# Optimization experiments

Hardware: AMD Instinct MI355X
Metric: run time of the kernel (lower is better)

Reference implementation:

```python
import jax, jax.numpy as jnp
import numpy as np

N_NODES = 100000
N_EDGES = 3200000
F_IN = 256
HIDDEN = 16
N_CLASSES = 32


def setup_inputs() -> dict:
    key = jax.random.key(0)
    ks = jax.random.split(key, 9)
    x = jax.random.normal(ks[0], (N_NODES, F_IN), dtype=jnp.float32)
    edge_index = jax.random.randint(ks[1], (2, N_EDGES), 0, N_NODES)
    edge_attr = jax.random.uniform(ks[2], (N_EDGES, 1), dtype=jnp.float32)
    s1 = 1.0 / np.sqrt(F_IN)
    W1 = jax.random.normal(ks[3], (2, F_IN, HIDDEN), dtype=jnp.float32) * s1
    root1 = jax.random.normal(ks[4], (F_IN, HIDDEN), dtype=jnp.float32) * s1
    bias1 = jnp.zeros((HIDDEN,), dtype=jnp.float32)
    s2 = 1.0 / np.sqrt(HIDDEN)
    W2 = jax.random.normal(ks[5], (2, HIDDEN, N_CLASSES), dtype=jnp.float32) * s2
    root2 = jax.random.normal(ks[6], (HIDDEN, N_CLASSES), dtype=jnp.float32) * s2
    bias2 = jnp.zeros((N_CLASSES,), dtype=jnp.float32)
    return {"x": x, "edge_attr": edge_attr, "W1": W1, "root1": root1,
            "bias1": bias1, "W2": W2, "root2": root2, "bias2": bias2,
            "edge_index": edge_index}


def spline_conv(x, src, dst, u, W, root, bias):
    """SplineConv, dim=1, kernel_size=2, degree=1, open spline, aggr='mean'.

    With K=2 and degree-1 open splines, v = u*(K-1) = u, so the B-spline basis
    per edge is simply ((1-u), u) over kernel weights W[0], W[1].
    """
    n = x.shape[0]
    # Node-level GEMMs once (cheaper than per-edge F_IN-dim gathers): [2, N, out]
    xs = jnp.einsum('nf,kfo->kno', x, W)
    # Per-edge basis-weighted message from source nodes: [E, out]
    msg = (1.0 - u)[:, None] * xs[0, src] + u[:, None] * xs[1, src]
    agg = jax.ops.segment_sum(msg, dst, num_segments=n)
    cnt = jax.ops.segment_sum(jnp.ones((dst.shape[0],), x.dtype), dst,
                              num_segments=n)
    return agg / jnp.maximum(cnt, 1.0)[:, None] + x @ root + bias


def reference(x, edge_attr, W1, root1, bias1, W2, root2, bias2, edge_index):
    src, dst = edge_index[0], edge_index[1]
    u = jnp.clip(edge_attr[:, 0], 0.0, 1.0)  # pseudo coords in [0, 1]
    # dropout with training=False is identity (eval-mode reference)
    h = jax.nn.elu(spline_conv(x, src, dst, u, W1, root1, bias1))
    out = spline_conv(h, src, dst, u, W2, root2, bias2)
    return jax.nn.log_softmax(out, axis=1)
```

## Files before the change

kernel.cpp:

```cpp
#include <hip/hip_runtime.h>
#include <hip/hip_fp16.h>
#include <math.h>

#define NN 100000
#define NE 3200000
#define FIN 256
#define HID 16
#define NC 32
#define NBUK 782
#define CAP 5120
#define SC_BLOCKS 250
#define SC_TILE 12800
#define SC_EPT 13
#define SK 20

typedef __attribute__((ext_vector_type(8))) short short8;
typedef __attribute__((ext_vector_type(4))) float f32x4;
typedef union { uint4 u; short8 s; } U8;

#define RU(r) ((float)((r) >> 24) * (1.f / 255.f))

__global__ __launch_bounds__(256) void k_prepB(
    const float* __restrict__ W1, const float* __restrict__ root1,
    uint4* __restrict__ Bpk)
{
    int idx = blockIdx.x * 256 + threadIdx.x;
    if (idx >= 1536) return;
    int c = idx & 15, kc = (idx >> 4) & 31, t = idx >> 9;
    unsigned hi[8], lo[8];
    #pragma unroll
    for (int e = 0; e < 8; ++e) {
        int k = kc * 8 + e;
        float v;
        if (t == 0)      v = W1[k * 16 + c];
        else if (t == 1) v = W1[FIN * 16 + k * 16 + c];
        else             v = root1[k * 16 + c];
        unsigned u = __float_as_uint(v);
        unsigned h = u & 0xFFFF0000u;
        float lf = v - __uint_as_float(h);
        hi[e] = h;
        lo[e] = __float_as_uint(lf) & 0xFFFF0000u;
    }
    uint4 H, L;
    H.x = (hi[0] >> 16) | hi[1];  H.y = (hi[2] >> 16) | hi[3];
    H.z = (hi[4] >> 16) | hi[5];  H.w = (hi[6] >> 16) | hi[7];
    L.x = (lo[0] >> 16) | lo[1];  L.y = (lo[2] >> 16) | lo[3];
    L.z = (lo[4] >> 16) | lo[5];  L.w = (lo[6] >> 16) | lo[7];
    Bpk[(size_t)idx * 2]     = H;
    Bpk[(size_t)idx * 2 + 1] = L;
}

__global__ __launch_bounds__(256) void k_gemm1(
    const float* __restrict__ x, const uint4* __restrict__ Bpk,
    const float* __restrict__ bias1,
    __half2* __restrict__ xs1p, __half2* __restrict__ r1h)
{
    int wid = (blockIdx.x << 2) + (threadIdx.x >> 6);
    if (wid >= NN / 16) return;
    int lane = threadIdx.x & 63;
    int c = lane & 15, kcl = lane >> 4;
    int n0 = wid * 16;

    const float* xr = x + (size_t)(n0 + c) * FIN + kcl * 8;
    f32x4 acc0 = {0.f, 0.f, 0.f, 0.f};
    f32x4 acc1 = {0.f, 0.f, 0.f, 0.f};
    f32x4 acc2 = {0.f, 0.f, 0.f, 0.f};

    #define PACK(f0, f1, HO, LO) {                                     \
        unsigned u0 = __float_as_uint(f0), u1 = __float_as_uint(f1);   \
        unsigned h0 = u0 & 0xFFFF0000u, h1 = u1 & 0xFFFF0000u;         \
        HO = (h0 >> 16) | h1;                                          \
        float l0 = (f0) - __uint_as_float(h0);                         \
        float l1 = (f1) - __uint_as_float(h1);                         \
        LO = (__float_as_uint(l0) >> 16) |                             \
             (__float_as_uint(l1) & 0xFFFF0000u); }

    #pragma unroll
    for (int s = 0; s < 8; ++s) {
        float4 a0 = *(const float4*)(xr + s * 32);
        float4 a1 = *(const float4*)(xr + s * 32 + 4);
        U8 ahi, alo;
        PACK(a0.x, a0.y, ahi.u.x, alo.u.x)
        PACK(a0.z, a0.w, ahi.u.y, alo.u.y)
        PACK(a1.x, a1.y, ahi.u.z, alo.u.z)
        PACK(a1.z, a1.w, ahi.u.w, alo.u.w)

        const uint4* bp = Bpk + ((size_t)((s * 4 + kcl) * 16 + c)) * 2;
        U8 bh0, bl0, bh1, bl1, bh2, bl2;
        bh0.u = bp[0];     bl0.u = bp[1];
        bh1.u = bp[1024];  bl1.u = bp[1025];
        bh2.u = bp[2048];  bl2.u = bp[2049];

        acc0 = __builtin_amdgcn_mfma_f32_16x16x32_bf16(ahi.s, bh0.s, acc0, 0, 0, 0);
        acc0 = __builtin_amdgcn_mfma_f32_16x16x32_bf16(alo.s, bh0.s, acc0, 0, 0, 0);
        acc0 = __builtin_amdgcn_mfma_f32_16x16x32_bf16(ahi.s, bl0.s, acc0, 0, 0, 0);
        acc1 = __builtin_amdgcn_mfma_f32_16x16x32_bf16(ahi.s, bh1.s, acc1, 0, 0, 0);
        acc1 = __builtin_amdgcn_mfma_f32_16x16x32_bf16(alo.s, bh1.s, acc1, 0, 0, 0);
        acc1 = __builtin_amdgcn_mfma_f32_16x16x32_bf16(ahi.s, bl1.s, acc1, 0, 0, 0);
        acc2 = __builtin_amdgcn_mfma_f32_16x16x32_bf16(ahi.s, bh2.s, acc2, 0, 0, 0);
        acc2 = __builtin_amdgcn_mfma_f32_16x16x32_bf16(alo.s, bh2.s, acc2, 0, 0, 0);
        acc2 = __builtin_amdgcn_mfma_f32_16x16x32_bf16(ahi.s, bl2.s, acc2, 0, 0, 0);
    }
    #undef PACK

    #pragma unroll
    for (int r = 0; r < 4; ++r) {
        int n = n0 + kcl * 4 + r;
        xs1p[(size_t)n * 16 + c] = __floats2half2_rn(acc0[r], acc1[r]);
    }
    float b = bias1[c];
    #pragma unroll
    for (int r = 0; r < 4; ++r) {
        int n = n0 + kcl * 4 + r;
        float v = acc2[r] + b;
        float vo = __shfl_xor(v, 1, 64);
        if (!(c & 1))
            r1h[(size_t)n * 8 + (c >> 1)] = __floats2half2_rn(v, vo);
    }
}

__global__ __launch_bounds__(1024) void k_binscatter(
    const int* __restrict__ ei, const float* __restrict__ ea,
    int* __restrict__ gcnt, unsigned* __restrict__ rec)
{
    __shared__ unsigned sbuf[SC_TILE];
    __shared__ int cnt[NBUK], gb[NBUK], cur[NBUK];
    __shared__ int ss[1024];
    int t = threadIdx.x;
    if (t < NBUK) cnt[t] = 0;
    __syncthreads();

    int e0 = blockIdx.x * SC_TILE;
    int   dl[SC_EPT];
    int   sl[SC_EPT];
    float ul[SC_EPT];
    #pragma unroll
    for (int k = 0; k < SC_EPT; ++k) {
        int i = t + k * 1024;
        if (i < SC_TILE) {
            dl[k] = ei[NE + e0 + i];
            sl[k] = ei[e0 + i];
            ul[k] = ea[e0 + i];
            atomicAdd(&cnt[dl[k] >> 7], 1);
        }
    }
    __syncthreads();

    int v = (t < NBUK) ? cnt[t] : 0;
    ss[t] = v;
    __syncthreads();
    for (int off = 1; off < 1024; off <<= 1) {
        int a = (t >= off) ? ss[t - off] : 0;
        __syncthreads();
        ss[t] += a;
        __syncthreads();
    }
    if (t < NBUK) {
        int lbase = ss[t] - v;
        cur[t] = lbase;
        if (v) gb[t] = t * CAP + atomicAdd(&gcnt[t], v) - lbase;
    }
    __syncthreads();

    #pragma unroll
    for (int k = 0; k < SC_EPT; ++k) {
        int i = t + k * 1024;
        if (i < SC_TILE) {
            float u = fminf(fmaxf(ul[k], 0.f), 1.f);
            unsigned uq = (unsigned)(u * 255.f + 0.5f);
            int pos = atomicAdd(&cur[dl[k] >> 7], 1);
            sbuf[pos] = (unsigned)sl[k] | ((unsigned)(dl[k] & 127) << 17)
                      | (uq << 24);
        }
    }
    __syncthreads();

    int wid = t >> 6, lane = t & 63;
    for (int b = wid; b < NBUK; b += 16) {
        int n_ = cnt[b];
        if (!n_) continue;
        int lb = cur[b] - n_;
        int gbb = gb[b];
        for (int i = lane; i < n_; i += 64)
            rec[gbb + lb + i] = sbuf[lb + i];
    }
}

__global__ __launch_bounds__(256) void k_sort(
    const int* __restrict__ gcnt, unsigned* __restrict__ rec,
    int* __restrict__ rstart, int* __restrict__ rend)
{
    __shared__ int cnt[128], cur[128], ss[128];
    int t = threadIdx.x;
    if (t < 128) cnt[t] = 0;
    __syncthreads();
    int start = blockIdx.x * CAP, m = gcnt[blockIdx.x];
    unsigned r[SK];
    int nr = 0;
    for (int i = start + t; i < start + m; i += 256) {
        unsigned v = rec[i];
        if (nr < SK) r[nr++] = v;
        atomicAdd(&cnt[(v >> 17) & 127], 1);
    }
    __syncthreads();
    if (t < 128) ss[t] = cnt[t];
    __syncthreads();
    for (int off = 1; off < 128; off <<= 1) {
        int a = (t < 128 && t >= off) ? ss[t - off] : 0;
        __syncthreads();
        if (t < 128) ss[t] += a;
        __syncthreads();
    }
    if (t < 128) {
        int excl = ss[t] - cnt[t];
        cur[t] = excl;
        int n = blockIdx.x * 128 + t;
        if (n < NN) {
            rstart[n] = start + excl;
            rend[n]   = start + excl + cnt[t];
        }
    }
    __syncthreads();
    for (int k = 0; k < nr; ++k) {
        int dl = (int)(r[k] >> 17) & 127;
        int p = atomicAdd(&cur[dl], 1);
        rec[start + p] = r[k];
    }
}

__global__ __launch_bounds__(256) void k_agg1g2(
    const int* __restrict__ rstart, const int* __restrict__ rend,
    const unsigned* __restrict__ rec, const uint4* __restrict__ xs4,
    const __half2* __restrict__ r1h, __half2* __restrict__ hh2)
{
    int t = threadIdx.x;
    int nl = t >> 2, j = t & 3;
    int n = blockIdx.x * 64 + nl;
    bool valid = n < NN;
    int s = 0, e = 0;
    if (valid) { s = rstart[n]; e = rend[n]; }
    int d = e - s;
    float a0 = 0.f, a1 = 0.f, a2 = 0.f, a3 = 0.f;

    #define ACC1(r_, g) {                                           \
        float u = RU(r_);                                           \
        float w0 = 1.f - u;                                         \
        const __half2* hp_ = (const __half2*)&(g);                  \
        float2 f0 = __half22float2(hp_[0]);                         \
        float2 f1 = __half22float2(hp_[1]);                         \
        float2 f2 = __half22float2(hp_[2]);                         \
        float2 f3 = __half22float2(hp_[3]);                         \
        a0 += w0 * f0.x + u * f0.y;                                 \
        a1 += w0 * f1.x + u * f1.y;                                 \
        a2 += w0 * f2.x + u * f2.y;                                 \
        a3 += w0 * f3.x + u * f3.y; }

    int k = s;
    for (; k + 8 <= e; k += 8) {
        unsigned q[8]; uint4 g[8];
        #pragma unroll
        for (int z = 0; z < 8; ++z) q[z] = rec[k + z];
        #pragma unroll
        for (int z = 0; z < 8; ++z) g[z] = xs4[(size_t)(q[z] & 0x1FFFF) * 4 + j];
        #pragma unroll
        for (int z = 0; z < 8; ++z) { ACC1(q[z], g[z]) }
    }
    for (; k < e; ++k) {
        unsigned q = rec[k];
        uint4 g = xs4[(size_t)(q & 0x1FFFF) * 4 + j];
        ACC1(q, g)
    }
    #undef ACC1

    if (valid) {
        float inv = 1.f / fmaxf((float)d, 1.f);
        float2 rrA = __half22float2(r1h[(size_t)n * 8 + 2 * j]);
        float2 rrB = __half22float2(r1h[(size_t)n * 8 + 2 * j + 1]);
        float v0 = a0 * inv + rrA.x;
        float v1 = a1 * inv + rrA.y;
        float v2 = a2 * inv + rrB.x;
        float v3 = a3 * inv + rrB.y;
        v0 = v0 > 0.f ? v0 : expm1f(v0);
        v1 = v1 > 0.f ? v1 : expm1f(v1);
        v2 = v2 > 0.f ? v2 : expm1f(v2);
        v3 = v3 > 0.f ? v3 : expm1f(v3);
        hh2[(size_t)n * 8 + 2 * j]     = __floats2half2_rn(v0, v1);
        hh2[(size_t)n * 8 + 2 * j + 1] = __floats2half2_rn(v2, v3);
    }
}

__global__ __launch_bounds__(256) void k_agg2(
    const int* __restrict__ rstart, const int* __restrict__ rend,
    const unsigned* __restrict__ rec, const uint2* __restrict__ hh,
    const float* __restrict__ W2, const float* __restrict__ root2,
    const float* __restrict__ bias2, float* __restrict__ out)
{
    __shared__ float wsm[1568];
    __shared__ float ssm[64 * 33];
    __shared__ float hv[64 * 18];
    int t = threadIdx.x;
    for (int i = t; i < 1568; i += 256)
        wsm[i] = (i < 1024) ? W2[i] : (i < 1536 ? root2[i - 1024] : bias2[i - 1536]);

    int nl = t >> 2, j = t & 3;
    int n = blockIdx.x * 64 + nl;
    bool valid = n < NN;
    int s = 0, e = 0;
    if (valid) { s = rstart[n]; e = rend[n]; }
    float s0[4] = {0.f, 0.f, 0.f, 0.f};
    float s1[4] = {0.f, 0.f, 0.f, 0.f};

    #define ACC2(r_, g) {                                           \
        float u = RU(r_);                                           \
        float w0 = 1.f - u;                                         \
        float2 f0 = __half22float2(*(const __half2*)&(g).x);        \
        float2 f1 = __half22float2(*(const __half2*)&(g).y);        \
        s0[0] += w0 * f0.x; s1[0] += u * f0.x;                      \
        s0[1] += w0 * f0.y; s1[1] += u * f0.y;                      \
        s0[2] += w0 * f1.x; s1[2] += u * f1.x;                      \
        s0[3] += w0 * f1.y; s1[3] += u * f1.y; }

    int k = s;
    for (; k + 8 <= e; k += 8) {
        unsigned q[8]; uint2 g[8];
        #pragma unroll
        for (int z = 0; z < 8; ++z) q[z] = rec[k + z];
        #pragma unroll
        for (int z = 0; z < 8; ++z) g[z] = hh[(size_t)(q[z] & 0x1FFFF) * 4 + j];
        #pragma unroll
        for (int z = 0; z < 8; ++z) { ACC2(q[z], g[z]) }
    }
    for (; k < e; ++k) {
        unsigned q = rec[k];
        uint2 g = hh[(size_t)(q & 0x1FFFF) * 4 + j];
        ACC2(q, g)
    }
    #undef ACC2

    float inv = 1.f / fmaxf((float)(e - s), 1.f);
    #pragma unroll
    for (int q2 = 0; q2 < 4; ++q2) {
        ssm[nl * 33 + 4 * j + q2] = s0[q2];
        ssm[nl * 33 + 16 + 4 * j + q2] = s1[q2];
    }
    if (valid) {
        uint2 gh = hh[(size_t)n * 4 + j];
        float2 h0 = __half22float2(*(const __half2*)&gh.x);
        float2 h1 = __half22float2(*(const __half2*)&gh.y);
        hv[nl * 18 + 4 * j]     = h0.x;
        hv[nl * 18 + 4 * j + 1] = h0.y;
        hv[nl * 18 + 4 * j + 2] = h1.x;
        hv[nl * 18 + 4 * j + 3] = h1.y;
    } else {
        hv[nl * 18 + 4 * j]     = 0.f;
        hv[nl * 18 + 4 * j + 1] = 0.f;
        hv[nl * 18 + 4 * j + 2] = 0.f;
        hv[nl * 18 + 4 * j + 3] = 0.f;
    }
    if (j == 0) hv[nl * 18 + 16] = inv;
    __syncthreads();

    float invn = hv[nl * 18 + 16];
    float v[8];
    #pragma unroll
    for (int cc = 0; cc < 8; ++cc) {
        int c = j * 8 + cc;
        float acc = wsm[1536 + c];
        float agg = 0.f;
        #pragma unroll
        for (int kk = 0; kk < 16; ++kk) {
            agg += ssm[nl * 33 + kk] * wsm[kk * 32 + c]
                 + ssm[nl * 33 + 16 + kk] * wsm[512 + kk * 32 + c];
            acc += hv[nl * 18 + kk] * wsm[1024 + kk * 32 + c];
        }
        v[cc] = acc + agg * invn;
    }

    float m = v[0];
    #pragma unroll
    for (int cc = 1; cc < 8; ++cc) m = fmaxf(m, v[cc]);
    #pragma unroll
    for (int off = 1; off < 4; off <<= 1)
        m = fmaxf(m, __shfl_xor(m, off, 4));
    float sm = 0.f;
    #pragma unroll
    for (int cc = 0; cc < 8; ++cc) sm += expf(v[cc] - m);
    #pragma unroll
    for (int off = 1; off < 4; off <<= 1)
        sm += __shfl_xor(sm, off, 4);
    float ls = m + logf(sm);
    if (valid) {
        float4* op = (float4*)(out + (size_t)n * 32 + j * 8);
        op[0] = make_float4(v[0] - ls, v[1] - ls, v[2] - ls, v[3] - ls);
        op[1] = make_float4(v[4] - ls, v[5] - ls, v[6] - ls, v[7] - ls);
    }
}

extern "C" void kernel_launch(void* const* d_in, const int* in_sizes, int n_in,
                              void* d_out, int out_size, void* d_ws, size_t ws_size,
                              hipStream_t stream)
{
    const float* x     = (const float*)d_in[0];
    const float* ea    = (const float*)d_in[1];
    const float* W1    = (const float*)d_in[2];
    const float* root1 = (const float*)d_in[3];
    const float* bias1 = (const float*)d_in[4];
    const float* W2    = (const float*)d_in[5];
    const float* root2 = (const float*)d_in[6];
    const float* bias2 = (const float*)d_in[7];
    const int*   ei    = (const int*)d_in[8];
    float* out = (float*)d_out;

    float* ws = (float*)d_ws;
    __half2* xs1p = (__half2*)ws;
    __half2* r1h  = (__half2*)(ws + (size_t)NN * 16);
    __half2* hh2  = (__half2*)(ws + (size_t)NN * 24);
    unsigned* rec = (unsigned*)(ws + (size_t)NN * 32);
    int*     iws  = (int*)(ws + (size_t)NN * 32 + (size_t)NBUK * CAP);
    int* rstart = iws;
    int* rend   = iws + NN;
    int* gcnt   = iws + 2 * NN;
    uint4* Bpk = (uint4*)(ws + (size_t)NN * 24);

    hipMemsetAsync(gcnt, 0, NBUK * sizeof(int), stream);

    k_prepB<<<6, 256, 0, stream>>>(W1, root1, Bpk);
    k_gemm1<<<(NN / 16 + 3) / 4, 256, 0, stream>>>(x, Bpk, bias1, xs1p, r1h);
    k_binscatter<<<SC_BLOCKS, 1024, 0, stream>>>(ei, ea, gcnt, rec);
    k_sort<<<NBUK, 256, 0, stream>>>(gcnt, rec, rstart, rend);
    k_agg1g2<<<(NN + 63) / 64, 256, 0, stream>>>(rstart, rend, rec,
                                                 (const uint4*)xs1p, r1h, hh2);
    k_agg2<<<(NN + 63) / 64, 256, 0, stream>>>(rstart, rend, rec,
                                               (const uint2*)hh2,
                                               W2, root2, bias2, out);
}
```

Before: 349.9 us.

## Fuse per-bucket counting sort into both aggregation kernels using shared memory

```diff
diff --git a/kernel.cpp b/kernel.cpp
--- a/kernel.cpp
+++ b/kernel.cpp
@@ -12,7 +12,6 @@
 #define SC_BLOCKS 250
 #define SC_TILE 12800
 #define SC_EPT 13
-#define SK 20
 
 typedef __attribute__((ext_vector_type(8))) short short8;
 typedef __attribute__((ext_vector_type(4))) float f32x4;
@@ -186,20 +185,23 @@
     }
 }
 
-__global__ __launch_bounds__(256) void k_sort(
-    const int* __restrict__ gcnt, unsigned* __restrict__ rec,
-    int* __restrict__ rstart, int* __restrict__ rend)
-{
+__global__ __launch_bounds__(512) void k_agg1s(
+    const int* __restrict__ gcnt, const unsigned* __restrict__ rec,
+    const uint4* __restrict__ xs4, const __half2* __restrict__ r1h,
+    __half2* __restrict__ hh2)
+{
+    __shared__ unsigned sa[CAP];
+    __shared__ unsigned sbv[CAP];
     __shared__ int cnt[128], cur[128], ss[128];
     int t = threadIdx.x;
     if (t < 128) cnt[t] = 0;
     __syncthreads();
-    int start = blockIdx.x * CAP, m = gcnt[blockIdx.x];
-    unsigned r[SK];
-    int nr = 0;
-    for (int i = start + t; i < start + m; i += 256) {
-        unsigned v = rec[i];
-        if (nr < SK) r[nr++] = v;
+
+    int b = blockIdx.x;
+    int base = b * CAP, m = gcnt[b];
+    for (int i = t; i < m; i += 512) {
+        unsigned v = rec[base + i];
+        sa[i] = v;
         atomicAdd(&cnt[(v >> 17) & 127], 1);
     }
     __syncthreads();
@@ -211,35 +213,18 @@
         if (t < 128) ss[t] += a;
         __syncthreads();
     }
-    if (t < 128) {
-        int excl = ss[t] - cnt[t];
-        cur[t] = excl;
-        int n = blockIdx.x * 128 + t;
-        if (n < NN) {
-            rstart[n] = start + excl;
-            rend[n]   = start + excl + cnt[t];
-        }
-    }
-    __syncthreads();
-    for (int k = 0; k < nr; ++k) {
-        int dl = (int)(r[k] >> 17) & 127;
-        int p = atomicAdd(&cur[dl], 1);
-        rec[start + p] = r[k];
-    }
-}
-
-__global__ __launch_bounds__(256) void k_agg1g2(
-    const int* __restrict__ rstart, const int* __restrict__ rend,
-    const unsigned* __restrict__ rec, const uint4* __restrict__ xs4,
-    const __half2* __restrict__ r1h, __half2* __restrict__ hh2)
-{
-    int t = threadIdx.x;
+    if (t < 128) cur[t] = ss[t] - cnt[t];
+    __syncthreads();
+    for (int i = t; i < m; i += 512) {
+        unsigned v = sa[i];
+        int p = atomicAdd(&cur[(v >> 17) & 127], 1);
+        sbv[p] = v;
+    }
+    __syncthreads();
+
     int nl = t >> 2, j = t & 3;
-    int n = blockIdx.x * 64 + nl;
-    bool valid = n < NN;
-    int s = 0, e = 0;
-    if (valid) { s = rstart[n]; e = rend[n]; }
-    int d = e - s;
+    int d = cnt[nl];
+    int s = cur[nl] - d, e = cur[nl];
     float a0 = 0.f, a1 = 0.f, a2 = 0.f, a3 = 0.f;
 
     #define ACC1(r_, g) {                                           \
@@ -259,20 +244,21 @@
     for (; k + 8 <= e; k += 8) {
         unsigned q[8]; uint4 g[8];
         #pragma unroll
-        for (int z = 0; z < 8; ++z) q[z] = rec[k + z];
+        for (int z = 0; z < 8; ++z) q[z] = sbv[k + z];
         #pragma unroll
         for (int z = 0; z < 8; ++z) g[z] = xs4[(size_t)(q[z] & 0x1FFFF) * 4 + j];
         #pragma unroll
         for (int z = 0; z < 8; ++z) { ACC1(q[z], g[z]) }
     }
     for (; k < e; ++k) {
-        unsigned q = rec[k];
+        unsigned q = sbv[k];
         uint4 g = xs4[(size_t)(q & 0x1FFFF) * 4 + j];
         ACC1(q, g)
     }
     #undef ACC1
 
-    if (valid) {
+    int n = b * 128 + nl;
+    if (n < NN) {
         float inv = 1.f / fmaxf((float)d, 1.f);
         float2 rrA = __half22float2(r1h[(size_t)n * 8 + 2 * j]);
         float2 rrB = __half22float2(r1h[(size_t)n * 8 + 2 * j + 1]);
@@ -289,24 +275,50 @@
     }
 }
 
-__global__ __launch_bounds__(256) void k_agg2(
-    const int* __restrict__ rstart, const int* __restrict__ rend,
-    const unsigned* __restrict__ rec, const uint2* __restrict__ hh,
-    const float* __restrict__ W2, const float* __restrict__ root2,
-    const float* __restrict__ bias2, float* __restrict__ out)
+__global__ __launch_bounds__(512) void k_agg2s(
+    const int* __restrict__ gcnt, const unsigned* __restrict__ rec,
+    const uint2* __restrict__ hh, const float* __restrict__ W2,
+    const float* __restrict__ root2, const float* __restrict__ bias2,
+    float* __restrict__ out)
 {
     __shared__ float wsm[1568];
-    __shared__ float ssm[64 * 33];
-    __shared__ float hv[64 * 18];
+    __shared__ unsigned sa[CAP];
+    __shared__ unsigned sbv[CAP];
+    __shared__ int cnt[128], cur[128], ss[128];
     int t = threadIdx.x;
-    for (int i = t; i < 1568; i += 256)
+    for (int i = t; i < 1568; i += 512)
         wsm[i] = (i < 1024) ? W2[i] : (i < 1536 ? root2[i - 1024] : bias2[i - 1536]);
+    if (t < 128) cnt[t] = 0;
+    __syncthreads();
+
+    int b = blockIdx.x;
+    int base = b * CAP, m = gcnt[b];
+    for (int i = t; i < m; i += 512) {
+        unsigned v = rec[base + i];
+        sa[i] = v;
+        atomicAdd(&cnt[(v >> 17) & 127], 1);
+    }
+    __syncthreads();
+    if (t < 128) ss[t] = cnt[t];
+    __syncthreads();
+    for (int off = 1; off < 128; off <<= 1) {
+        int a = (t < 128 && t >= off) ? ss[t - off] : 0;
+        __syncthreads();
+        if (t < 128) ss[t] += a;
+        __syncthreads();
+    }
+    if (t < 128) cur[t] = ss[t] - cnt[t];
+    __syncthreads();
+    for (int i = t; i < m; i += 512) {
+        unsigned v = sa[i];
+        int p = atomicAdd(&cur[(v >> 17) & 127], 1);
+        sbv[p] = v;
+    }
+    __syncthreads();
 
     int nl = t >> 2, j = t & 3;
-    int n = blockIdx.x * 64 + nl;
-    bool valid = n < NN;
-    int s = 0, e = 0;
-    if (valid) { s = rstart[n]; e = rend[n]; }
+    int d = cnt[nl];
+    int s = cur[nl] - d, e = cur[nl];
     float s0[4] = {0.f, 0.f, 0.f, 0.f};
     float s1[4] = {0.f, 0.f, 0.f, 0.f};
 
@@ -324,25 +336,30 @@
     for (; k + 8 <= e; k += 8) {
         unsigned q[8]; uint2 g[8];
         #pragma unroll
-        for (int z = 0; z < 8; ++z) q[z] = rec[k + z];
+        for (int z = 0; z < 8; ++z) q[z] = sbv[k + z];
         #pragma unroll
         for (int z = 0; z < 8; ++z) g[z] = hh[(size_t)(q[z] & 0x1FFFF) * 4 + j];
         #pragma unroll
         for (int z = 0; z < 8; ++z) { ACC2(q[z], g[z]) }
     }
     for (; k < e; ++k) {
-        unsigned q = rec[k];
+        unsigned q = sbv[k];
         uint2 g = hh[(size_t)(q & 0x1FFFF) * 4 + j];
         ACC2(q, g)
     }
     #undef ACC2
 
-    float inv = 1.f / fmaxf((float)(e - s), 1.f);
+    float* ssm = (float*)sa;
     #pragma unroll
     for (int q2 = 0; q2 < 4; ++q2) {
         ssm[nl * 33 + 4 * j + q2] = s0[q2];
         ssm[nl * 33 + 16 + 4 * j + q2] = s1[q2];
     }
+    __syncthreads();
+
+    float* hv = (float*)sbv;
+    int n = b * 128 + nl;
+    bool valid = n < NN;
     if (valid) {
         uint2 gh = hh[(size_t)n * 4 + j];
         float2 h0 = __half22float2(*(const __half2*)&gh.x);
@@ -357,7 +374,7 @@
         hv[nl * 18 + 4 * j + 2] = 0.f;
         hv[nl * 18 + 4 * j + 3] = 0.f;
     }
-    if (j == 0) hv[nl * 18 + 16] = inv;
+    if (j == 0) hv[nl * 18 + 16] = 1.f / fmaxf((float)d, 1.f);
     __syncthreads();
 
     float invn = hv[nl * 18 + 16];
@@ -376,19 +393,19 @@
         v[cc] = acc + agg * invn;
     }
 
-    float m = v[0];
-    #pragma unroll
-    for (int cc = 1; cc < 8; ++cc) m = fmaxf(m, v[cc]);
+    float mx = v[0];
+    #pragma unroll
+    for (int cc = 1; cc < 8; ++cc) mx = fmaxf(mx, v[cc]);
     #pragma unroll
     for (int off = 1; off < 4; off <<= 1)
-        m = fmaxf(m, __shfl_xor(m, off, 4));
+        mx = fmaxf(mx, __shfl_xor(mx, off, 4));
     float sm = 0.f;
     #pragma unroll
-    for (int cc = 0; cc < 8; ++cc) sm += expf(v[cc] - m);
+    for (int cc = 0; cc < 8; ++cc) sm += expf(v[cc] - mx);
     #pragma unroll
     for (int off = 1; off < 4; off <<= 1)
         sm += __shfl_xor(sm, off, 4);
-    float ls = m + logf(sm);
+    float ls = mx + logf(sm);
     if (valid) {
         float4* op = (float4*)(out + (size_t)n * 32 + j * 8);
         op[0] = make_float4(v[0] - ls, v[1] - ls, v[2] - ls, v[3] - ls);
@@ -416,10 +433,7 @@
     __half2* r1h  = (__half2*)(ws + (size_t)NN * 16);
     __half2* hh2  = (__half2*)(ws + (size_t)NN * 24);
     unsigned* rec = (unsigned*)(ws + (size_t)NN * 32);
-    int*     iws  = (int*)(ws + (size_t)NN * 32 + (size_t)NBUK * CAP);
-    int* rstart = iws;
-    int* rend   = iws + NN;
-    int* gcnt   = iws + 2 * NN;
+    int*     gcnt = (int*)(ws + (size_t)NN * 32 + (size_t)NBUK * CAP);
     uint4* Bpk = (uint4*)(ws + (size_t)NN * 24);
 
     hipMemsetAsync(gcnt, 0, NBUK * sizeof(int), stream);
@@ -427,10 +441,7 @@
     k_prepB<<<6, 256, 0, stream>>>(W1, root1, Bpk);
     k_gemm1<<<(NN / 16 + 3) / 4, 256, 0, stream>>>(x, Bpk, bias1, xs1p, r1h);
     k_binscatter<<<SC_BLOCKS, 1024, 0, stream>>>(ei, ea, gcnt, rec);
-    k_sort<<<NBUK, 256, 0, stream>>>(gcnt, rec, rstart, rend);
-    k_agg1g2<<<(NN + 63) / 64, 256, 0, stream>>>(rstart, rend, rec,
-                                                 (const uint4*)xs1p, r1h, hh2);
-    k_agg2<<<(NN + 63) / 64, 256, 0, stream>>>(rstart, rend, rec,
-                                               (const uint2*)hh2,
-                                               W2, root2, bias2, out);
-}
+    k_agg1s<<<NBUK, 512, 0, stream>>>(gcnt, rec, (const uint4*)xs1p, r1h, hh2);
+    k_agg2s<<<NBUK, 512, 0, stream>>>(gcnt, rec, (const uint2*)hh2,
+                                      W2, root2, bias2, out);
+}
```

New measurement: 339.3 us. 3.0% less time.
